# Performance work log

Measured on AMD Instinct MI355X. Metric: run time of the kernel, lower is better.

## Reference

```python
import jax, jax.numpy as jnp
import numpy as np

N_USERS = 300000
N_ITEMS = 200000
N = N_USERS + N_ITEMS   # total nodes
E = 1250000             # edges
DIM = 64
N_LAYERS = 3


def setup_inputs() -> dict:
    key = jax.random.key(0)
    k1, k2, k3 = jax.random.split(key, 3)
    # xavier-uniform-ish init for embedding table
    bound = float(np.sqrt(6.0 / (N + DIM)))
    embedding = jax.random.uniform(k1, (N, DIM), dtype=jnp.float32, minval=-bound, maxval=bound)
    edge_index = jax.random.randint(k2, (2, E), 0, N, dtype=jnp.int64)
    edge_weight = jax.random.uniform(k3, (E,), dtype=jnp.float32)
    return {"embedding": embedding, "edge_index": edge_index, "edge_weight": edge_weight}


def reference(embedding, edge_index, edge_weight):
    # LightGCN propagation: L layers of gather-scale-scatter_add, mean over layers 0..L
    row, col = edge_index[0], edge_index[1]
    x = embedding
    acc = embedding  # layer-0 embedding contributes to the mean
    for _ in range(N_LAYERS):
        # agg[col] += edge_weight * x[row]  (SpMM over sparse edges)
        msgs = edge_weight[:, None] * x[row]          # [E, DIM]
        x = jax.ops.segment_sum(msgs, col, num_segments=N)  # [N, DIM]
        acc = acc + x
    return acc / jnp.float32(N_LAYERS + 1)
```

## Files before the change

kernel.cpp:

```cpp
#include <hip/hip_runtime.h>


#define NNODES   500000
#define DIMV     64
#define NEDGE    1250000
#define NELEM    (NNODES * DIMV)
#define NELEM4   (NELEM / 4)

#define SCAN_BLK   256
#define SCAN_ITEMS 8
#define SCAN_CHUNK (SCAN_BLK * SCAN_ITEMS)
#define NB1 ((NNODES + SCAN_CHUNK - 1) / SCAN_CHUNK)

#define CVT_BLOCKS  1024
#define EDGE2_BLOCKS ((NEDGE / 2 + 255) / 256)

typedef float  fx4 __attribute__((ext_vector_type(4)));
typedef unsigned ux4 __attribute__((ext_vector_type(4)));

static __device__ __forceinline__ unsigned short f2bf(float f) {
    unsigned u = __float_as_uint(f);
    unsigned r = (u + 0x7fffu + ((u >> 16) & 1u)) >> 16;
    return (unsigned short)r;
}
static __device__ __forceinline__ float bflo(unsigned u) {
    return __uint_as_float(u << 16);
}
static __device__ __forceinline__ float bfhi(unsigned u) {
    return __uint_as_float(u & 0xffff0000u);
}

__global__ __launch_bounds__(256) void lgcn_cvt_hist(
    const float4* __restrict__ emb4, unsigned long long* __restrict__ dst,
    const int* __restrict__ col, int* __restrict__ cnt)
{
    if (blockIdx.x < CVT_BLOCKS) {
        int i = blockIdx.x * 256 + threadIdx.x;
        const int stride = CVT_BLOCKS * 256;
        for (; i < NELEM4; i += stride) {
            float4 v = emb4[i];
            unsigned lo = (unsigned)f2bf(v.x) | ((unsigned)f2bf(v.y) << 16);
            unsigned hi = (unsigned)f2bf(v.z) | ((unsigned)f2bf(v.w) << 16);
            unsigned long long o = (unsigned long long)lo | ((unsigned long long)hi << 32);
            __builtin_nontemporal_store(o, &dst[i]);
        }
    } else {
        int t = (blockIdx.x - CVT_BLOCKS) * 256 + threadIdx.x;
        if (t >= NEDGE / 2) return;
        int2 c2 = reinterpret_cast<const int2*>(col)[t];
        if ((unsigned)c2.x < NNODES) atomicAdd(&cnt[c2.x], 1);
        if ((unsigned)c2.y < NNODES) atomicAdd(&cnt[c2.y], 1);
    }
}


__global__ __launch_bounds__(SCAN_BLK) void lgcn_scan1(
    const int* __restrict__ cnt, int* __restrict__ startv, int* __restrict__ bsum)
{
    __shared__ int sh[SCAN_BLK];
    int b = blockIdx.x;
    int base = b * SCAN_CHUNK;
    int tid = threadIdx.x;
    int v[SCAN_ITEMS];
    int local = 0;
    #pragma unroll
    for (int k = 0; k < SCAN_ITEMS; ++k) {
        int idx = base + tid * SCAN_ITEMS + k;
        v[k] = (idx < NNODES) ? cnt[idx] : 0;
        local += v[k];
    }
    sh[tid] = local;
    __syncthreads();
    for (int off = 1; off < SCAN_BLK; off <<= 1) {
        int x = (tid >= off) ? sh[tid - off] : 0;
        __syncthreads();
        sh[tid] += x;
        __syncthreads();
    }
    int run = (tid == 0) ? 0 : sh[tid - 1];
    if (tid == SCAN_BLK - 1) bsum[b] = sh[tid];
    #pragma unroll
    for (int k = 0; k < SCAN_ITEMS; ++k) {
        int idx = base + tid * SCAN_ITEMS + k;
        if (idx < NNODES) startv[idx] = run;
        run += v[k];
    }
}

__global__ __launch_bounds__(SCAN_BLK) void lgcn_scan2(int* __restrict__ bsum)
{
    __shared__ int sh[SCAN_BLK];
    int tid = threadIdx.x;
    sh[tid] = (tid < NB1) ? bsum[tid] : 0;
    __syncthreads();
    for (int off = 1; off < SCAN_BLK; off <<= 1) {
        int x = (tid >= off) ? sh[tid - off] : 0;
        __syncthreads();
        sh[tid] += x;
        __syncthreads();
    }
    if (tid < NB1) bsum[tid] = (tid == 0) ? 0 : sh[tid - 1];
}

__global__ __launch_bounds__(256) void lgcn_scan3(
    int* __restrict__ startv, int* __restrict__ cursor, const int* __restrict__ bsum)
{
    int i = blockIdx.x * blockDim.x + threadIdx.x;
    if (i < NNODES) {
        int s = startv[i] + bsum[i / SCAN_CHUNK];
        startv[i] = s;
        cursor[i] = s;
    }
    if (i == 0) startv[NNODES] = NEDGE;
}

__global__ __launch_bounds__(256) void lgcn_fill(
    const int* __restrict__ row, const int* __restrict__ col,
    const float* __restrict__ w, int* __restrict__ cursor,
    unsigned long long* __restrict__ pairs)
{
    int t = blockIdx.x * blockDim.x + threadIdx.x;
    if (t >= NEDGE / 2) return;
    int2   c2 = reinterpret_cast<const int2*>(col)[t];
    int2   r2 = reinterpret_cast<const int2*>(row)[t];
    float2 w2 = reinterpret_cast<const float2*>(w)[t];

    if ((unsigned)c2.x < NNODES) {
        int r = r2.x; float wt = w2.x;
        if ((unsigned)r >= NNODES) { r = 0; wt = 0.f; }
        int p = atomicAdd(&cursor[c2.x], 1);
        unsigned long long pk = (unsigned long long)(unsigned)r
                              | ((unsigned long long)__float_as_uint(wt) << 32);
        __builtin_nontemporal_store(pk, &pairs[p]);
    }
    if ((unsigned)c2.y < NNODES) {
        int r = r2.y; float wt = w2.y;
        if ((unsigned)r >= NNODES) { r = 0; wt = 0.f; }
        int p = atomicAdd(&cursor[c2.y], 1);
        unsigned long long pk = (unsigned long long)(unsigned)r
                              | ((unsigned long long)__float_as_uint(wt) << 32);
        __builtin_nontemporal_store(pk, &pairs[p]);
    }
}

template<int MODE>
__global__ __launch_bounds__(256, 4) void lgcn_gather(
    const unsigned short* __restrict__ src16, unsigned short* __restrict__ xout16,
    const float* __restrict__ emb, const unsigned short* __restrict__ x1,
    const unsigned short* __restrict__ x2, float* __restrict__ outp,
    const int2* __restrict__ pairs, const int* __restrict__ startv)
{
    int t = blockIdx.x * blockDim.x + threadIdx.x;
    int wid = t >> 6;
    int lane = t & 63;
    int g = lane >> 3;
    int sub = lane & 7;
    int n = wid * 8 + g;
    if (n >= NNODES) return;

    int s = startv[n];
    int e = startv[n + 1];

    float a0=0.f,a1=0.f,a2=0.f,a3=0.f,a4=0.f,a5=0.f,a6=0.f,a7=0.f;

    for (int i = s; i < e; i += 8) {
        int2 pr[8];
        #pragma unroll
        for (int k = 0; k < 8; ++k) {
            int idx = i + k;
            idx = idx < e ? idx : e - 1;
            pr[k] = pairs[idx];
        }
        uint4 rv[8];
        #pragma unroll
        for (int k = 0; k < 8; ++k) {
            rv[k] = *reinterpret_cast<const uint4*>(
                &src16[(size_t)pr[k].x * DIMV + sub * 8]);
        }
        #pragma unroll
        for (int k = 0; k < 8; ++k) {
            float wk = (i + k < e) ? __int_as_float(pr[k].y) : 0.f;
            a0 = fmaf(wk, bflo(rv[k].x), a0);
            a1 = fmaf(wk, bfhi(rv[k].x), a1);
            a2 = fmaf(wk, bflo(rv[k].y), a2);
            a3 = fmaf(wk, bfhi(rv[k].y), a3);
            a4 = fmaf(wk, bflo(rv[k].z), a4);
            a5 = fmaf(wk, bfhi(rv[k].z), a5);
            a6 = fmaf(wk, bflo(rv[k].w), a6);
            a7 = fmaf(wk, bfhi(rv[k].w), a7);
        }
    }

    const size_t o = (size_t)n * DIMV + sub * 8;
    if (MODE == 2) {
        fx4 e0 = __builtin_nontemporal_load(reinterpret_cast<const fx4*>(&emb[o]));
        fx4 e1 = __builtin_nontemporal_load(reinterpret_cast<const fx4*>(&emb[o + 4]));
        ux4 u1 = __builtin_nontemporal_load(reinterpret_cast<const ux4*>(&x1[o]));
        uint4 u2 = *reinterpret_cast<const uint4*>(&x2[o]);
        fx4 r0, r1;
        r0.x = (e0.x + bflo(u1.x) + bflo(u2.x) + a0) * 0.25f;
        r0.y = (e0.y + bfhi(u1.x) + bfhi(u2.x) + a1) * 0.25f;
        r0.z = (e0.z + bflo(u1.y) + bflo(u2.y) + a2) * 0.25f;
        r0.w = (e0.w + bfhi(u1.y) + bfhi(u2.y) + a3) * 0.25f;
        r1.x = (e1.x + bflo(u1.z) + bflo(u2.z) + a4) * 0.25f;
        r1.y = (e1.y + bfhi(u1.z) + bfhi(u2.z) + a5) * 0.25f;
        r1.z = (e1.z + bflo(u1.w) + bflo(u2.w) + a6) * 0.25f;
        r1.w = (e1.w + bfhi(u1.w) + bfhi(u2.w) + a7) * 0.25f;
        __builtin_nontemporal_store(r0, reinterpret_cast<fx4*>(&outp[o]));
        __builtin_nontemporal_store(r1, reinterpret_cast<fx4*>(&outp[o + 4]));
    } else {
        unsigned long long lo =
              (unsigned long long)((unsigned)f2bf(a0) | ((unsigned)f2bf(a1) << 16))
            | ((unsigned long long)((unsigned)f2bf(a2) | ((unsigned)f2bf(a3) << 16)) << 32);
        unsigned long long hi =
              (unsigned long long)((unsigned)f2bf(a4) | ((unsigned)f2bf(a5) << 16))
            | ((unsigned long long)((unsigned)f2bf(a6) | ((unsigned)f2bf(a7) << 16)) << 32);
        __builtin_nontemporal_store(lo, reinterpret_cast<unsigned long long*>(&xout16[o]));
        __builtin_nontemporal_store(hi, reinterpret_cast<unsigned long long*>(&xout16[o + 4]));
    }
}


__global__ __launch_bounds__(256) void lgcn_init(
    const float4* __restrict__ emb, float4* __restrict__ acc,
    float4* __restrict__ A, float4* __restrict__ B)
{
    int i = blockIdx.x * blockDim.x + threadIdx.x;
    int stride = gridDim.x * blockDim.x;
    for (; i < NELEM4; i += stride) {
        float4 v = emb[i];
        acc[i] = v;
        A[i]   = v;
        B[i]   = make_float4(0.f, 0.f, 0.f, 0.f);
    }
}

__global__ __launch_bounds__(256) void lgcn_scatter(
    const float* __restrict__ xcur, float* __restrict__ xnext,
    const int* __restrict__ row, const int* __restrict__ col,
    const float* __restrict__ w)
{
    int t = blockIdx.x * blockDim.x + threadIdx.x;
    int e = t >> 4;
    if (e >= NEDGE) return;
    int d = (t & 15) << 2;
    int r = row[e];
    int c = col[e];
    if ((unsigned)r >= NNODES || (unsigned)c >= NNODES) return;
    float wt = w[e];
    const float4 v = *reinterpret_cast<const float4*>(xcur + (size_t)r * DIMV + d);
    float* dst = xnext + (size_t)c * DIMV + d;
    atomicAdd(dst + 0, wt * v.x);
    atomicAdd(dst + 1, wt * v.y);
    atomicAdd(dst + 2, wt * v.z);
    atomicAdd(dst + 3, wt * v.w);
}

__global__ __launch_bounds__(256) void lgcn_addzero(
    float4* __restrict__ acc, const float4* __restrict__ X, float4* __restrict__ Y)
{
    int i = blockIdx.x * blockDim.x + threadIdx.x;
    int stride = gridDim.x * blockDim.x;
    for (; i < NELEM4; i += stride) {
        float4 a = acc[i];
        float4 x = X[i];
        a.x += x.x; a.y += x.y; a.z += x.z; a.w += x.w;
        acc[i] = a;
        Y[i] = make_float4(0.f, 0.f, 0.f, 0.f);
    }
}

__global__ __launch_bounds__(256) void lgcn_final(
    float4* __restrict__ acc, const float4* __restrict__ X)
{
    int i = blockIdx.x * blockDim.x + threadIdx.x;
    int stride = gridDim.x * blockDim.x;
    for (; i < NELEM4; i += stride) {
        float4 a = acc[i];
        float4 x = X[i];
        a.x = (a.x + x.x) * 0.25f;
        a.y = (a.y + x.y) * 0.25f;
        a.z = (a.z + x.z) * 0.25f;
        a.w = (a.w + x.w) * 0.25f;
        acc[i] = a;
    }
}


extern "C" void kernel_launch(void* const* d_in, const int* in_sizes, int n_in,
                              void* d_out, int out_size, void* d_ws, size_t ws_size,
                              hipStream_t stream) {
    const float* emb  = (const float*)d_in[0];
    const int*   eidx = (const int*)d_in[1];
    const float* ew   = (const float*)d_in[2];
    float* acc = (float*)d_out;

    const int* row = eidx;
    const int* col = eidx + NEDGE;

    unsigned short* E16 = (unsigned short*)d_ws;
    unsigned short* X1  = E16 + NELEM;
    unsigned short* X2  = X1 + NELEM;
    int2*  pairs  = (int2*)(X2 + NELEM);
    int*   startv = (int*)(pairs + NEDGE);
    int*   cursor = startv + (NNODES + 1);
    int*   bsum   = cursor + NNODES;
    const size_t needed = (size_t)3 * NELEM * 2 + (size_t)NEDGE * 8
                        + ((size_t)NNODES + 1) * 4 + (size_t)NNODES * 4 + (size_t)NB1 * 4;

    const int NODE_BLOCKS = (NNODES + 255) / 256;
    const int GW_BLOCKS   = (NNODES * 8 + 255) / 256;

    if (ws_size >= needed) {
        hipMemsetAsync(cursor, 0, (size_t)NNODES * 4, stream);
        lgcn_cvt_hist<<<CVT_BLOCKS + EDGE2_BLOCKS, 256, 0, stream>>>(
            (const float4*)emb, (unsigned long long*)E16, col, cursor);

        lgcn_scan1<<<NB1, SCAN_BLK, 0, stream>>>(cursor, startv, bsum);
        lgcn_scan2<<<1, SCAN_BLK, 0, stream>>>(bsum);
        lgcn_scan3<<<NODE_BLOCKS, 256, 0, stream>>>(startv, cursor, bsum);
        lgcn_fill<<<EDGE2_BLOCKS, 256, 0, stream>>>(
            row, col, ew, cursor, (unsigned long long*)pairs);

        lgcn_gather<0><<<GW_BLOCKS, 256, 0, stream>>>(
            E16, X1, nullptr, nullptr, nullptr, nullptr, pairs, startv);
        lgcn_gather<1><<<GW_BLOCKS, 256, 0, stream>>>(
            X1, X2, nullptr, nullptr, nullptr, nullptr, pairs, startv);
        lgcn_gather<2><<<GW_BLOCKS, 256, 0, stream>>>(
            X2, nullptr, emb, X1, X2, acc, pairs, startv);
    } else {
        float* A = (float*)d_ws;
        float* B = A + NELEM;
        const int SC_BLOCKS = (NEDGE * 16 + 255) / 256;
        lgcn_init<<<2048, 256, 0, stream>>>(
            (const float4*)emb, (float4*)acc, (float4*)A, (float4*)B);
        lgcn_scatter<<<SC_BLOCKS, 256, 0, stream>>>(A, B, row, col, ew);
        lgcn_addzero<<<2048, 256, 0, stream>>>((float4*)acc, (const float4*)B, (float4*)A);
        lgcn_scatter<<<SC_BLOCKS, 256, 0, stream>>>(B, A, row, col, ew);
        lgcn_addzero<<<2048, 256, 0, stream>>>((float4*)acc, (const float4*)A, (float4*)B);
        lgcn_scatter<<<SC_BLOCKS, 256, 0, stream>>>(A, B, row, col, ew);
        lgcn_final<<<2048, 256, 0, stream>>>((float4*)acc, (const float4*)B);
    }
}
```

Baseline: 381.6 us.

## Partition CSR fill by destination column range across block classes

```diff
diff --git a/kernel.cpp b/kernel.cpp
--- a/kernel.cpp
+++ b/kernel.cpp
@@ -14,6 +14,10 @@
 
 #define CVT_BLOCKS  1024
 #define EDGE2_BLOCKS ((NEDGE / 2 + 255) / 256)
+
+#define FILL_CLASSES  8
+#define FILL_BPC      256
+#define COLS_PER_CLS  (NNODES / FILL_CLASSES)
 
 typedef float  fx4 __attribute__((ext_vector_type(4)));
 typedef unsigned ux4 __attribute__((ext_vector_type(4)));
@@ -114,32 +118,35 @@
     if (i == 0) startv[NNODES] = NEDGE;
 }
 
-__global__ __launch_bounds__(256) void lgcn_fill(
+__global__ __launch_bounds__(256) void lgcn_fill_part(
     const int* __restrict__ row, const int* __restrict__ col,
     const float* __restrict__ w, int* __restrict__ cursor,
     unsigned long long* __restrict__ pairs)
 {
-    int t = blockIdx.x * blockDim.x + threadIdx.x;
-    if (t >= NEDGE / 2) return;
-    int2   c2 = reinterpret_cast<const int2*>(col)[t];
-    int2   r2 = reinterpret_cast<const int2*>(row)[t];
-    float2 w2 = reinterpret_cast<const float2*>(w)[t];
-
-    if ((unsigned)c2.x < NNODES) {
-        int r = r2.x; float wt = w2.x;
-        if ((unsigned)r >= NNODES) { r = 0; wt = 0.f; }
-        int p = atomicAdd(&cursor[c2.x], 1);
-        unsigned long long pk = (unsigned long long)(unsigned)r
-                              | ((unsigned long long)__float_as_uint(wt) << 32);
-        __builtin_nontemporal_store(pk, &pairs[p]);
-    }
-    if ((unsigned)c2.y < NNODES) {
-        int r = r2.y; float wt = w2.y;
-        if ((unsigned)r >= NNODES) { r = 0; wt = 0.f; }
-        int p = atomicAdd(&cursor[c2.y], 1);
-        unsigned long long pk = (unsigned long long)(unsigned)r
-                              | ((unsigned long long)__float_as_uint(wt) << 32);
-        __builtin_nontemporal_store(pk, &pairs[p]);
+    const int cls = blockIdx.x & (FILL_CLASSES - 1);
+    const int q   = blockIdx.x >> 3;
+    const int lo  = cls * COLS_PER_CLS;
+    const int hi  = lo + COLS_PER_CLS;
+    const int2* col2 = reinterpret_cast<const int2*>(col);
+
+    for (int t = q * 256 + threadIdx.x; t < NEDGE / 2; t += FILL_BPC * 256) {
+        int2 c2 = col2[t];
+        if (c2.x >= lo && c2.x < hi) {
+            int e = 2 * t;
+            int r = row[e]; float wt = w[e];
+            if ((unsigned)r >= NNODES) { r = 0; wt = 0.f; }
+            int p = atomicAdd(&cursor[c2.x], 1);
+            pairs[p] = (unsigned long long)(unsigned)r
+                     | ((unsigned long long)__float_as_uint(wt) << 32);
+        }
+        if (c2.y >= lo && c2.y < hi) {
+            int e = 2 * t + 1;
+            int r = row[e]; float wt = w[e];
+            if ((unsigned)r >= NNODES) { r = 0; wt = 0.f; }
+            int p = atomicAdd(&cursor[c2.y], 1);
+            pairs[p] = (unsigned long long)(unsigned)r
+                     | ((unsigned long long)__float_as_uint(wt) << 32);
+        }
     }
 }
 
@@ -319,7 +326,7 @@
         lgcn_scan1<<<NB1, SCAN_BLK, 0, stream>>>(cursor, startv, bsum);
         lgcn_scan2<<<1, SCAN_BLK, 0, stream>>>(bsum);
         lgcn_scan3<<<NODE_BLOCKS, 256, 0, stream>>>(startv, cursor, bsum);
-        lgcn_fill<<<EDGE2_BLOCKS, 256, 0, stream>>>(
+        lgcn_fill_part<<<FILL_CLASSES * FILL_BPC, 256, 0, stream>>>(
             row, col, ew, cursor, (unsigned long long*)pairs);
 
         lgcn_gather<0><<<GW_BLOCKS, 256, 0, stream>>>(
```

New measurement: 349.0 us. 1.09x faster.
